# Kernel optimization log

Hardware: AMD Instinct MI355X
Metric: run time of the kernel (lower is better)

## Reference

```python
import jax, jax.numpy as jnp
import numpy as np

N_NODES = 100000
N_EDGES = 1600000
IN_DIM, HID_DIM, OUT_DIM = 256, 64, 64


def gcn_conv(x, src, dst, W, b, n_nodes):
    """PyG GCNConv: D^-1/2 (A + I) D^-1/2 X W + b (self-loops added, deg on dst)."""
    h = x @ W  # [N, D_out]
    ones = jnp.ones(src.shape[0], dtype=h.dtype)
    deg = jax.ops.segment_sum(ones, dst, num_segments=n_nodes) + 1.0  # +1 for self-loop
    dinv = jax.lax.rsqrt(deg)  # deg >= 1, always finite
    norm = dinv[src] * dinv[dst]  # [E]
    # neighbor aggregation (scatter-add) + self-loop contribution
    agg = jax.ops.segment_sum(h[src] * norm[:, None], dst, num_segments=n_nodes)
    agg = agg + h * (dinv * dinv)[:, None]
    return agg + b


def gcn_backbone(x, edge_index, W1, b1, W2, b2, n_nodes):
    src, dst = edge_index[0], edge_index[1]
    h = jax.nn.relu(gcn_conv(x, src, dst, W1, b1, n_nodes))
    h = gcn_conv(h, src, dst, W2, b2, n_nodes)
    return h


def zscore(h):
    # torch .std(0) is unbiased (ddof=1)
    return (h - h.mean(axis=0)) / jnp.std(h, axis=0, ddof=1)


def setup_inputs() -> dict:
    key = jax.random.key(0)
    k = jax.random.split(key, 8)
    x1 = jax.random.normal(k[0], (N_NODES, IN_DIM), dtype=jnp.float32)
    x2 = jax.random.normal(k[1], (N_NODES, IN_DIM), dtype=jnp.float32)
    edge_index1 = jax.random.randint(k[2], (2, N_EDGES), 0, N_NODES, dtype=jnp.int64)
    edge_index2 = jax.random.randint(k[3], (2, N_EDGES), 0, N_NODES, dtype=jnp.int64)
    W1 = jax.random.normal(k[4], (IN_DIM, HID_DIM), dtype=jnp.float32) * (1.0 / np.sqrt(IN_DIM))
    b1 = jnp.zeros((HID_DIM,), dtype=jnp.float32)
    W2 = jax.random.normal(k[5], (HID_DIM, OUT_DIM), dtype=jnp.float32) * (1.0 / np.sqrt(HID_DIM))
    b2 = jnp.zeros((OUT_DIM,), dtype=jnp.float32)
    return {"x1": x1, "edge_index1": edge_index1, "x2": x2, "edge_index2": edge_index2,
            "W1": W1, "b1": b1, "W2": W2, "b2": b2}


def reference(x1, edge_index1, x2, edge_index2, W1, b1, W2, b2):
    h1 = gcn_backbone(x1, edge_index1, W1, b1, W2, b2, N_NODES)
    h2 = gcn_backbone(x2, edge_index2, W1, b1, W2, b2, N_NODES)
    return zscore(h1), zscore(h2)
```

## Files before the change

### kernel.cpp

```cpp
#include <hip/hip_runtime.h>
#include <hip/hip_bf16.h>

#define HD 64
#define CH 8192
#define BKT_SHIFT 10
#define SRC_BITS 17
#define MAXBLK 256

typedef __attribute__((ext_vector_type(8))) short bf16x8;
typedef __attribute__((ext_vector_type(4))) float f32x4;
typedef __attribute__((ext_vector_type(4))) unsigned int u32x4;

#define WAITALL do { asm volatile("s_waitcnt vmcnt(0)" ::: "memory"); \
                     __builtin_amdgcn_sched_barrier(0); } while (0)

__device__ inline unsigned short f2bf(float x) {
  unsigned u = __float_as_uint(x);
  unsigned r = u + 0x7FFF + ((u >> 16) & 1);
  return (unsigned short)(r >> 16);
}
__device__ inline float bf2f(unsigned short h) {
  return __uint_as_float(((unsigned)h) << 16);
}

__global__ __launch_bounds__(256) void k_wprep(const float* __restrict__ W1,
                                               const float* __restrict__ W2,
                                               unsigned short* __restrict__ Wf1,
                                               unsigned short* __restrict__ Wf2hi,
                                               unsigned short* __restrict__ Wf2lo) {
  int idx = blockIdx.x * blockDim.x + threadIdx.x;
  if (idx < 256 * 64) {
    int k = idx >> 6, c = idx & 63;
    float w = W1[idx];
    int ks = k >> 5, r = k & 31, h2 = r >> 3, j = r & 7;
    int f = c >> 4, r16c = c & 15;
    int pos = (((ks * 4 + f) * 64) + h2 * 16 + r16c) * 8 + j;
    Wf1[pos] = f2bf(w);
  } else if (idx < 256 * 64 + 64 * 64) {
    int i2 = idx - 256 * 64;
    int k = i2 >> 6, c = i2 & 63;
    float w = W2[i2];
    int ks = k >> 5, r = k & 31, h2 = r >> 3, j = r & 7;
    int f = c >> 4, r16c = c & 15;
    int pos = (((ks * 4 + f) * 64) + h2 * 16 + r16c) * 8 + j;
    unsigned short hi = f2bf(w);
    Wf2hi[pos] = hi;
    Wf2lo[pos] = f2bf(w - bf2f(hi));
  }
}

__global__ __launch_bounds__(256) void k_front(
    const float* __restrict__ X0, const float* __restrict__ X1,
    const unsigned short* __restrict__ Wf1, unsigned short* __restrict__ Hb,
    int N, int gPer,
    const int* __restrict__ srcA, const int* __restrict__ dstA,
    const int* __restrict__ srcB, const int* __restrict__ dstB,
    int* __restrict__ tmp, int* __restrict__ counts, int* __restrict__ offsets,
    int NB, int NBLK, int E) {
  __shared__ int hist[128];
  __shared__ int pref[128];
  __shared__ int lofs[128];
  __shared__ int stage[CH];
  const int tid = threadIdx.x;
  const int bid = blockIdx.x;
  const int nGemm = 2 * gPer;

  if (bid < nGemm) {
    const int g = bid / gPer;
    const int bblk = bid % gPer;
    const float* __restrict__ Xv = g ? X1 : X0;
    const int lane = tid & 63;
    const int wv = tid >> 6;
    const int r16 = lane & 15;
    const int half = lane >> 4;
    const int row = bblk * 64 + wv * 16 + r16;
    const int rowc = min(row, N - 1);

    unsigned long long xa =
        (unsigned long long)(const void*)(Xv + (size_t)rowc * 256 + half * 8);
    f32x4 a[16];
    asm volatile(
        "global_load_dwordx4 %0, %16, off\n\t"
        "global_load_dwordx4 %1, %16, off offset:16\n\t"
        "global_load_dwordx4 %2, %16, off offset:128\n\t"
        "global_load_dwordx4 %3, %16, off offset:144\n\t"
        "global_load_dwordx4 %4, %16, off offset:256\n\t"
        "global_load_dwordx4 %5, %16, off offset:272\n\t"
        "global_load_dwordx4 %6, %16, off offset:384\n\t"
        "global_load_dwordx4 %7, %16, off offset:400\n\t"
        "global_load_dwordx4 %8, %16, off offset:512\n\t"
        "global_load_dwordx4 %9, %16, off offset:528\n\t"
        "global_load_dwordx4 %10, %16, off offset:640\n\t"
        "global_load_dwordx4 %11, %16, off offset:656\n\t"
        "global_load_dwordx4 %12, %16, off offset:768\n\t"
        "global_load_dwordx4 %13, %16, off offset:784\n\t"
        "global_load_dwordx4 %14, %16, off offset:896\n\t"
        "global_load_dwordx4 %15, %16, off offset:912\n\t"
        : "=&v"(a[0]), "=&v"(a[1]), "=&v"(a[2]), "=&v"(a[3]), "=&v"(a[4]),
          "=&v"(a[5]), "=&v"(a[6]), "=&v"(a[7]), "=&v"(a[8]), "=&v"(a[9]),
          "=&v"(a[10]), "=&v"(a[11]), "=&v"(a[12]), "=&v"(a[13]), "=&v"(a[14]),
          "=&v"(a[15])
        : "v"(xa));

    const unsigned long long wb = (unsigned long long)(const void*)Wf1 + lane * 16;
    bf16x8 B[32];
    asm volatile(
        "global_load_dwordx4 %0, %16, off\n\t"
        "global_load_dwordx4 %1, %16, off offset:1024\n\t"
        "global_load_dwordx4 %2, %16, off offset:2048\n\t"
        "global_load_dwordx4 %3, %16, off offset:3072\n\t"
        "global_load_dwordx4 %4, %17, off\n\t"
        "global_load_dwordx4 %5, %17, off offset:1024\n\t"
        "global_load_dwordx4 %6, %17, off offset:2048\n\t"
        "global_load_dwordx4 %7, %17, off offset:3072\n\t"
        "global_load_dwordx4 %8, %18, off\n\t"
        "global_load_dwordx4 %9, %18, off offset:1024\n\t"
        "global_load_dwordx4 %10, %18, off offset:2048\n\t"
        "global_load_dwordx4 %11, %18, off offset:3072\n\t"
        "global_load_dwordx4 %12, %19, off\n\t"
        "global_load_dwordx4 %13, %19, off offset:1024\n\t"
        "global_load_dwordx4 %14, %19, off offset:2048\n\t"
        "global_load_dwordx4 %15, %19, off offset:3072\n\t"
        : "=&v"(B[0]), "=&v"(B[1]), "=&v"(B[2]), "=&v"(B[3]), "=&v"(B[4]),
          "=&v"(B[5]), "=&v"(B[6]), "=&v"(B[7]), "=&v"(B[8]), "=&v"(B[9]),
          "=&v"(B[10]), "=&v"(B[11]), "=&v"(B[12]), "=&v"(B[13]), "=&v"(B[14]),
          "=&v"(B[15])
        : "v"(wb), "v"(wb + 4096), "v"(wb + 8192), "v"(wb + 12288));

    WAITALL;

    asm volatile(
        "global_load_dwordx4 %0, %16, off\n\t"
        "global_load_dwordx4 %1, %16, off offset:1024\n\t"
        "global_load_dwordx4 %2, %16, off offset:2048\n\t"
        "global_load_dwordx4 %3, %16, off offset:3072\n\t"
        "global_load_dwordx4 %4, %17, off\n\t"
        "global_load_dwordx4 %5, %17, off offset:1024\n\t"
        "global_load_dwordx4 %6, %17, off offset:2048\n\t"
        "global_load_dwordx4 %7, %17, off offset:3072\n\t"
        "global_load_dwordx4 %8, %18, off\n\t"
        "global_load_dwordx4 %9, %18, off offset:1024\n\t"
        "global_load_dwordx4 %10, %18, off offset:2048\n\t"
        "global_load_dwordx4 %11, %18, off offset:3072\n\t"
        "global_load_dwordx4 %12, %19, off\n\t"
        "global_load_dwordx4 %13, %19, off offset:1024\n\t"
        "global_load_dwordx4 %14, %19, off offset:2048\n\t"
        "global_load_dwordx4 %15, %19, off offset:3072\n\t"
        : "=&v"(B[16]), "=&v"(B[17]), "=&v"(B[18]), "=&v"(B[19]), "=&v"(B[20]),
          "=&v"(B[21]), "=&v"(B[22]), "=&v"(B[23]), "=&v"(B[24]), "=&v"(B[25]),
          "=&v"(B[26]), "=&v"(B[27]), "=&v"(B[28]), "=&v"(B[29]), "=&v"(B[30]),
          "=&v"(B[31])
        : "v"(wb + 16384), "v"(wb + 20480), "v"(wb + 24576), "v"(wb + 28672));

    f32x4 acc[4];
#pragma unroll
    for (int f = 0; f < 4; ++f) acc[f] = (f32x4){0.f, 0.f, 0.f, 0.f};

#pragma unroll
    for (int ks = 0; ks < 4; ++ks) {
      union { __hip_bfloat162 h[4]; bf16x8 v; } cu;
      cu.h[0] = __float22bfloat162_rn(make_float2(a[2 * ks][0], a[2 * ks][1]));
      cu.h[1] = __float22bfloat162_rn(make_float2(a[2 * ks][2], a[2 * ks][3]));
      cu.h[2] = __float22bfloat162_rn(make_float2(a[2 * ks + 1][0], a[2 * ks + 1][1]));
      cu.h[3] = __float22bfloat162_rn(make_float2(a[2 * ks + 1][2], a[2 * ks + 1][3]));
#pragma unroll
      for (int f = 0; f < 4; ++f)
        acc[f] = __builtin_amdgcn_mfma_f32_16x16x32_bf16(cu.v, B[ks * 4 + f], acc[f], 0, 0, 0);
    }

    WAITALL;

#pragma unroll
    for (int ks = 4; ks < 8; ++ks) {
      union { __hip_bfloat162 h[4]; bf16x8 v; } cu;
      cu.h[0] = __float22bfloat162_rn(make_float2(a[2 * ks][0], a[2 * ks][1]));
      cu.h[1] = __float22bfloat162_rn(make_float2(a[2 * ks][2], a[2 * ks][3]));
      cu.h[2] = __float22bfloat162_rn(make_float2(a[2 * ks + 1][0], a[2 * ks + 1][1]));
      cu.h[3] = __float22bfloat162_rn(make_float2(a[2 * ks + 1][2], a[2 * ks + 1][3]));
#pragma unroll
      for (int f = 0; f < 4; ++f)
        acc[f] = __builtin_amdgcn_mfma_f32_16x16x32_bf16(cu.v, B[ks * 4 + f], acc[f], 0, 0, 0);
    }

    const int orow0 = bblk * 64 + wv * 16 + half * 4;
#pragma unroll
    for (int f = 0; f < 4; ++f) {
#pragma unroll
      for (int rg = 0; rg < 4; ++rg) {
        int orow = orow0 + rg;
        if (orow < N) Hb[((size_t)g * N + orow) * HD + f * 16 + r16] = f2bf(acc[f][rg]);
      }
    }
    return;
  }

  const int blk2 = bid - nGemm;
  const int g = blk2 / NBLK;
  const int blk = blk2 % NBLK;
  const int* __restrict__ src = g ? srcB : srcA;
  const int* __restrict__ dst = g ? dstB : dstA;
  int* __restrict__ tmpg = tmp + (size_t)g * NBLK * CH;
  int* __restrict__ cntg = counts + (size_t)g * NB * NBLK;
  int* __restrict__ offg = offsets + (size_t)g * NB * NBLK;
  const int e0 = blk * CH;
  const int len = min(CH, E - e0);
  const int t = tid;

  for (int i = t; i < 128; i += 256) hist[i] = 0;
  __syncthreads();
  int dreg[CH / 256];
#pragma unroll
  for (int it = 0; it < CH / 256; ++it) {
    int i = t + it * 256;
    if (i < len) {
      int d = dst[e0 + i];
      dreg[it] = d;
      atomicAdd(&hist[d >> BKT_SHIFT], 1);
    }
  }
  __syncthreads();
  if (t < 128) pref[t] = hist[t];
  __syncthreads();
  for (int off = 1; off < 128; off <<= 1) {
    int v = 0;
    if (t < 128 && t >= off) v = pref[t - off];
    __syncthreads();
    if (t < 128) pref[t] += v;
    __syncthreads();
  }
  if (t < NB) {
    int ex = pref[t] - hist[t];
    lofs[t] = ex;
    cntg[t * NBLK + blk] = hist[t];
    offg[t * NBLK + blk] = ex;
  }
  __syncthreads();
#pragma unroll
  for (int it = 0; it < CH / 256; ++it) {
    int i = t + it * 256;
    if (i < len) {
      int d = dreg[it], s = src[e0 + i];
      int slot = atomicAdd(&lofs[d >> BKT_SHIFT], 1);
      stage[slot] = ((d & ((1 << BKT_SHIFT) - 1)) << SRC_BITS) | s;
    }
  }
  __syncthreads();
  int nv = len >> 2;
  for (int i = t; i < nv; i += 256) ((int4*)(tmpg + e0))[i] = ((const int4*)stage)[i];
  for (int i = (nv << 2) + t; i < len; i += 256) tmpg[e0 + i] = stage[i];
}

__global__ __launch_bounds__(128) void k_bscan(const int* __restrict__ counts,
                                               int* __restrict__ bucket_base,
                                               int* __restrict__ row_start,
                                               int NB, int NBLK, int N, int E) {
  __shared__ int sh[128];
  const int g = blockIdx.x;
  const int* __restrict__ cntg = counts + (size_t)g * NB * NBLK;
  int* __restrict__ bbg = bucket_base + g * (NB + 1);
  int* __restrict__ rsg = row_start + (size_t)g * (N + 1);
  int t = threadIdx.x;
  int v = 0;
  if (t < NB) {
    const int* p = cntg + t * NBLK;
    for (int i = 0; i < NBLK; ++i) v += p[i];
  }
  sh[t] = v;
  __syncthreads();
  for (int off = 1; off < 128; off <<= 1) {
    int x = (t >= off) ? sh[t - off] : 0;
    __syncthreads();
    sh[t] += x;
    __syncthreads();
  }
  if (t < NB) bbg[t] = sh[t] - v;
  if (t == 0) {
    bbg[NB] = E;
    rsg[N] = E;
  }
}

__global__ __launch_bounds__(1024) void k_bin2m(const int* __restrict__ tmp,
                                                const int* __restrict__ counts,
                                                const int* __restrict__ offsets,
                                                const int* __restrict__ bucket_base,
                                                int* __restrict__ row_start,
                                                float* __restrict__ dinv,
                                                int* __restrict__ recs, int N, int NB,
                                                int NBLK, int E) {
  __shared__ int h[1 << BKT_SHIFT];
  __shared__ int lcur[1 << BKT_SHIFT];
  __shared__ int scnt[MAXBLK], soff[MAXBLK];
  const int g = blockIdx.x / NB;
  const int b = blockIdx.x % NB;
  const int* __restrict__ tmpg = tmp + (size_t)g * NBLK * CH;
  const int* __restrict__ cntg = counts + (size_t)g * NB * NBLK;
  const int* __restrict__ offg = offsets + (size_t)g * NB * NBLK;
  const int* __restrict__ bbg = bucket_base + g * (NB + 1);
  int* __restrict__ rsg = row_start + (size_t)g * (N + 1);
  float* __restrict__ dig = dinv + (size_t)g * N;
  int* __restrict__ recg = recs + (size_t)g * E;
  const int t = threadIdx.x;
  const int node0 = b << BKT_SHIFT;
  const int lane = t & 63, w = t >> 6;

  h[t] = 0;
  for (int i = t; i < NBLK; i += 1024) {
    scnt[i] = cntg[b * NBLK + i];
    soff[i] = offg[b * NBLK + i];
  }
  __syncthreads();
  for (int blk = w; blk < NBLK; blk += 16) {
    int cnt = scnt[blk];
    const int* p = tmpg + blk * CH + soff[blk];
    for (int j = lane; j < cnt; j += 64) atomicAdd(&h[p[j] >> SRC_BITS], 1);
  }
  __syncthreads();
  int deg = h[t];
  __syncthreads();
  for (int off = 1; off < 1024; off <<= 1) {
    int x = (t >= off) ? h[t - off] : 0;
    __syncthreads();
    h[t] += x;
    __syncthreads();
  }
  int base = bbg[b] + h[t] - deg;
  lcur[t] = base;
  int n = node0 + t;
  if (n < N) {
    rsg[n] = base;
    dig[n] = rsqrtf((float)deg + 1.0f);
  }
  __syncthreads();
  for (int blk = w; blk < NBLK; blk += 16) {
    int cnt = scnt[blk];
    const int* p = tmpg + blk * CH + soff[blk];
    for (int j = lane; j < cnt; j += 64) {
      int rec = p[j];
      int d = rec >> SRC_BITS;
      int s = rec & ((1 << SRC_BITS) - 1);
      int slot = atomicAdd(&lcur[d], 1);
      recg[slot] = s;
    }
  }
}

__global__ __launch_bounds__(256) void k_gemm2(const unsigned short* __restrict__ Xb,
                                               const unsigned short* __restrict__ Wfh,
                                               const unsigned short* __restrict__ Wfl,
                                               unsigned short* __restrict__ Hb, int M) {
  const int tid = threadIdx.x;
  const int row0 = blockIdx.x * 64;
  const int lane = tid & 63;
  const int wv = tid >> 6;
  const int r16 = lane & 15;
  const int half = lane >> 4;
  const int row = row0 + wv * 16 + r16;
  const int rowc = min(row, M - 1);

  unsigned long long xa =
      (unsigned long long)(const void*)(Xb + (size_t)rowc * 64 + half * 8);
  const unsigned long long bh = (unsigned long long)(const void*)Wfh + lane * 16;
  const unsigned long long bl = (unsigned long long)(const void*)Wfl + lane * 16;
  u32x4 A0, A1;
  bf16x8 BH[8], BL[8];
  asm volatile(
      "global_load_dwordx4 %0, %18, off\n\t"
      "global_load_dwordx4 %1, %18, off offset:64\n\t"
      "global_load_dwordx4 %2, %19, off\n\t"
      "global_load_dwordx4 %3, %19, off offset:1024\n\t"
      "global_load_dwordx4 %4, %19, off offset:2048\n\t"
      "global_load_dwordx4 %5, %19, off offset:3072\n\t"
      "global_load_dwordx4 %6, %20, off\n\t"
      "global_load_dwordx4 %7, %20, off offset:1024\n\t"
      "global_load_dwordx4 %8, %20, off offset:2048\n\t"
      "global_load_dwordx4 %9, %20, off offset:3072\n\t"
      "global_load_dwordx4 %10, %21, off\n\t"
      "global_load_dwordx4 %11, %21, off offset:1024\n\t"
      "global_load_dwordx4 %12, %21, off offset:2048\n\t"
      "global_load_dwordx4 %13, %21, off offset:3072\n\t"
      "global_load_dwordx4 %14, %22, off\n\t"
      "global_load_dwordx4 %15, %22, off offset:1024\n\t"
      "global_load_dwordx4 %16, %22, off offset:2048\n\t"
      "global_load_dwordx4 %17, %22, off offset:3072\n\t"
      : "=&v"(A0), "=&v"(A1), "=&v"(BH[0]), "=&v"(BH[1]), "=&v"(BH[2]),
        "=&v"(BH[3]), "=&v"(BH[4]), "=&v"(BH[5]), "=&v"(BH[6]), "=&v"(BH[7]),
        "=&v"(BL[0]), "=&v"(BL[1]), "=&v"(BL[2]), "=&v"(BL[3]), "=&v"(BL[4]),
        "=&v"(BL[5]), "=&v"(BL[6]), "=&v"(BL[7])
      : "v"(xa), "v"(bh), "v"(bh + 4096), "v"(bl), "v"(bl + 4096));

  WAITALL;

  f32x4 acc[4];
#pragma unroll
  for (int f = 0; f < 4; ++f) acc[f] = (f32x4){0.f, 0.f, 0.f, 0.f};

  union { u32x4 u; bf16x8 v; } a0u, a1u;
  a0u.u = A0;
  a1u.u = A1;
#pragma unroll
  for (int f = 0; f < 4; ++f) {
    acc[f] = __builtin_amdgcn_mfma_f32_16x16x32_bf16(a0u.v, BH[f], acc[f], 0, 0, 0);
    acc[f] = __builtin_amdgcn_mfma_f32_16x16x32_bf16(a0u.v, BL[f], acc[f], 0, 0, 0);
    acc[f] = __builtin_amdgcn_mfma_f32_16x16x32_bf16(a1u.v, BH[4 + f], acc[f], 0, 0, 0);
    acc[f] = __builtin_amdgcn_mfma_f32_16x16x32_bf16(a1u.v, BL[4 + f], acc[f], 0, 0, 0);
  }

  const int orow0 = row0 + wv * 16 + half * 4;
#pragma unroll
  for (int f = 0; f < 4; ++f) {
#pragma unroll
    for (int rg = 0; rg < 4; ++rg) {
      int orow = orow0 + rg;
      if (orow < M) Hb[(size_t)orow * HD + f * 16 + r16] = f2bf(acc[f][rg]);
    }
  }
}

template <int OUTBF16>
__global__ __launch_bounds__(256) void k_agg(const unsigned short* __restrict__ Hb,
                                             const int* __restrict__ recs,
                                             const int* __restrict__ row_start,
                                             const float* __restrict__ dinv,
                                             const float* __restrict__ bias,
                                             void* __restrict__ outv, int N, int E,
                                             int relu) {
  const int t = threadIdx.x;
  const int nglob = (blockIdx.x * blockDim.x + t) >> 4;
  const int lane16 = t & 15;
  if (nglob >= 2 * N) return;
  const int g = nglob >= N;
  const int node = nglob - g * N;
  const int* __restrict__ rsg = row_start + (size_t)g * (N + 1);
  const int* __restrict__ R = recs + (size_t)g * E;
  const float* __restrict__ dig = dinv + (size_t)g * N;
  const unsigned short* __restrict__ Hbg = Hb + (size_t)g * N * HD;

  const int c0 = lane16 * 4;
  float di = dig[node];
  float a0, a1, a2, a3;
  {
    uint2 h = *(const uint2*)&Hbg[(size_t)node * HD + c0];
    float dd = di * di;
    a0 = bf2f((unsigned short)(h.x & 0xffff)) * dd;
    a1 = bf2f((unsigned short)(h.x >> 16)) * dd;
    a2 = bf2f((unsigned short)(h.y & 0xffff)) * dd;
    a3 = bf2f((unsigned short)(h.y >> 16)) * dd;
  }
  const int beg = rsg[node], end = rsg[node + 1];
  int e = beg;
  for (; e + 8 <= end; e += 8) {
    int s[8];
    uint2 gg[8];
    float n[8];
#pragma unroll
    for (int j = 0; j < 8; ++j) s[j] = R[e + j];
#pragma unroll
    for (int j = 0; j < 8; ++j) {
      gg[j] = *(const uint2*)&Hbg[(size_t)s[j] * HD + c0];
      n[j] = dig[s[j]];
    }
#pragma unroll
    for (int j = 0; j < 8; ++j) {
      float nn = n[j] * di;
      a0 = fmaf(bf2f((unsigned short)(gg[j].x & 0xffff)), nn, a0);
      a1 = fmaf(bf2f((unsigned short)(gg[j].x >> 16)), nn, a1);
      a2 = fmaf(bf2f((unsigned short)(gg[j].y & 0xffff)), nn, a2);
      a3 = fmaf(bf2f((unsigned short)(gg[j].y >> 16)), nn, a3);
    }
  }
  for (; e < end; ++e) {
    int s = R[e];
    uint2 gg = *(const uint2*)&Hbg[(size_t)s * HD + c0];
    float nn = dig[s] * di;
    a0 = fmaf(bf2f((unsigned short)(gg.x & 0xffff)), nn, a0);
    a1 = fmaf(bf2f((unsigned short)(gg.x >> 16)), nn, a1);
    a2 = fmaf(bf2f((unsigned short)(gg.y & 0xffff)), nn, a2);
    a3 = fmaf(bf2f((unsigned short)(gg.y >> 16)), nn, a3);
  }
  float4 bv = *(const float4*)&bias[c0];
  a0 += bv.x; a1 += bv.y; a2 += bv.z; a3 += bv.w;
  if (relu) {
    a0 = fmaxf(a0, 0.f); a1 = fmaxf(a1, 0.f);
    a2 = fmaxf(a2, 0.f); a3 = fmaxf(a3, 0.f);
  }
  if (OUTBF16) {
    uint2 o;
    o.x = ((unsigned)f2bf(a1) << 16) | f2bf(a0);
    o.y = ((unsigned)f2bf(a3) << 16) | f2bf(a2);
    *(uint2*)&((unsigned short*)outv)[(size_t)nglob * HD + c0] = o;
  } else {
    *(float4*)&((float*)outv)[(size_t)nglob * HD + c0] = make_float4(a0, a1, a2, a3);
  }
}


__global__ void k_colstats(const float* __restrict__ H, float* __restrict__ stats, int N,
                           int gridPer) {
  __shared__ float ss[256], sq[256];
  const int g = blockIdx.x / gridPer;
  const int blk = blockIdx.x % gridPer;
  const float* __restrict__ Hg = H + (size_t)g * N * HD;
  float* __restrict__ st = stats + g * 128;
  int t = threadIdx.x;
  int col = t & 63, grp = t >> 6;
  float s = 0.f, q = 0.f;
  for (int row = blk * 4 + grp; row < N; row += gridPer * 4) {
    float v = Hg[(size_t)row * HD + col];
    s += v;
    q += v * v;
  }
  ss[t] = s;
  sq[t] = q;
  __syncthreads();
  if (t < 64) {
    s = ss[t] + ss[t + 64] + ss[t + 128] + ss[t + 192];
    q = sq[t] + sq[t + 64] + sq[t + 128] + sq[t + 192];
    atomicAdd(&st[t], s);
    atomicAdd(&st[64 + t], q);
  }
}

__global__ void k_normalize(float* __restrict__ H, const float* __restrict__ stats, int N) {
  int i = blockIdx.x * blockDim.x + threadIdx.x;
  int total = 2 * N * HD;
  if (i >= total) return;
  int col = i & 63;
  const float* st = stats + (i >= N * HD ? 128 : 0);
  float sum = st[col], sumsq = st[64 + col];
  float mean = sum / (float)N;
  float var = (sumsq - sum * sum / (float)N) / (float)(N - 1);
  float r = rsqrtf(var);
  H[i] = (H[i] - mean) * r;
}


extern "C" void kernel_launch(void* const* d_in, const int* in_sizes, int n_in,
                              void* d_out, int out_size, void* d_ws, size_t ws_size,
                              hipStream_t stream) {
  const int IN_DIM = 256;
  const float* X1 = (const float*)d_in[0];
  const float* X2 = (const float*)d_in[2];
  const int* EI1 = (const int*)d_in[1];
  const int* EI2 = (const int*)d_in[3];
  const float* W1 = (const float*)d_in[4];
  const float* b1 = (const float*)d_in[5];
  const float* W2 = (const float*)d_in[6];
  const float* b2 = (const float*)d_in[7];
  const int N = in_sizes[0] / IN_DIM;
  const int E = in_sizes[1] / 2;
  const int NB = (N + (1 << BKT_SHIFT) - 1) >> BKT_SHIFT;
  const int NBLK = (E + CH - 1) / CH;

  char* ws = (char*)d_ws;
  size_t off = 0;
  auto carve = [&](size_t bytes) -> char* {
    char* p = ws + off;
    off += (bytes + 255) & ~(size_t)255;
    return p;
  };
  unsigned short* Hb = (unsigned short*)carve((size_t)2 * N * HD * 2);
  int* tmp = (int*)carve((size_t)2 * NBLK * CH * 4);
  int* recs = (int*)carve((size_t)2 * E * 4);
  char* zero_base = carve(256 * 4);
  float* stats = (float*)zero_base;
  int* row_start = (int*)carve((size_t)2 * (N + 1) * 4);
  float* dinv = (float*)carve((size_t)2 * N * 4);
  int* bucket_base = (int*)carve((size_t)2 * (NB + 1) * 4);
  int* counts = (int*)carve((size_t)2 * NB * NBLK * 4);
  int* offsets = (int*)carve((size_t)2 * NB * NBLK * 4);
  unsigned short* Wf1 = (unsigned short*)carve(256 * 64 * 2);
  unsigned short* Wf2hi = (unsigned short*)carve(64 * 64 * 2);
  unsigned short* Wf2lo = (unsigned short*)carve(64 * 64 * 2);
  unsigned short* bufAgg = (unsigned short*)d_out;
  (void)ws_size; (void)n_in; (void)out_size;

  const int T = 256;
  const int gPer1 = (N + 63) / 64;
  const int gG2 = (2 * N + 63) / 64;
  const int gAgg = (2 * N * 16 + T - 1) / T;
  const int gCS = 512;
  const int gElem = (2 * N * HD + T - 1) / T;
  const int gWp = (256 * 64 + 64 * 64 + T - 1) / T;

  (void)hipMemsetAsync(zero_base, 0, 256 * 4, stream);
  k_wprep<<<gWp, T, 0, stream>>>(W1, W2, Wf1, Wf2hi, Wf2lo);
  k_front<<<2 * gPer1 + 2 * NBLK, T, 0, stream>>>(X1, X2, Wf1, Hb, N, gPer1,
                                                  EI1, EI1 + E, EI2, EI2 + E,
                                                  tmp, counts, offsets, NB, NBLK, E);
  k_bscan<<<2, 128, 0, stream>>>(counts, bucket_base, row_start, NB, NBLK, N, E);
  k_bin2m<<<2 * NB, 1024, 0, stream>>>(tmp, counts, offsets, bucket_base, row_start,
                                       dinv, recs, N, NB, NBLK, E);

  k_agg<1><<<gAgg, T, 0, stream>>>(Hb, recs, row_start, dinv, b1, bufAgg, N, E, 1);
  k_gemm2<<<gG2, T, 0, stream>>>(bufAgg, Wf2hi, Wf2lo, Hb, 2 * N);
  k_agg<0><<<gAgg, T, 0, stream>>>(Hb, recs, row_start, dinv, b2, d_out, N, E, 0);

  k_colstats<<<2 * gCS, T, 0, stream>>>((float*)d_out, stats, N, gCS);
  k_normalize<<<gElem, T, 0, stream>>>((float*)d_out, stats, N);
}
```

Measured before the change: 364.3 us.

## Fuse column statistics into the final aggregation and interleave GEMM with binning blocks

The separate column-statistics kernel is removed. The second aggregation kernel now accumulates per-column sums and sums of squares in shared memory with atomics, then flushes them to global stats once per block. This avoids a full re-read of the fp32 output. The front kernel also interleaves edge-binning blocks among the GEMM blocks, one in every eight, instead of placing them after all GEMM blocks, so the memory-bound binning runs alongside the compute-heavy GEMM. The cost is shared-memory atomic contention and an extra barrier in the aggregation kernel.

```diff
diff --git a/kernel.cpp b/kernel.cpp
--- a/kernel.cpp
+++ b/kernel.cpp
@@ -63,11 +63,15 @@
   __shared__ int stage[CH];
   const int tid = threadIdx.x;
   const int bid = blockIdx.x;
-  const int nGemm = 2 * gPer;
-
-  if (bid < nGemm) {
-    const int g = bid / gPer;
-    const int bblk = bid % gPer;
+  const int nBin = 2 * NBLK;
+
+  const int q = bid >> 3, r8 = bid & 7;
+  const bool isBin = (r8 == 7) && (q < nBin);
+
+  if (!isBin) {
+    const int gemmIdx = bid - min(nBin, (bid + 1) >> 3);
+    const int g = gemmIdx / gPer;
+    const int bblk = gemmIdx % gPer;
     const float* __restrict__ Xv = g ? X1 : X0;
     const int lane = tid & 63;
     const int wv = tid >> 6;
@@ -194,9 +198,8 @@
     return;
   }
 
-  const int blk2 = bid - nGemm;
-  const int g = blk2 / NBLK;
-  const int blk = blk2 % NBLK;
+  const int g = q / NBLK;
+  const int blk = q % NBLK;
   const int* __restrict__ src = g ? srcB : srcA;
   const int* __restrict__ dst = g ? dstB : dstA;
   int* __restrict__ tmpg = tmp + (size_t)g * NBLK * CH;
@@ -417,109 +420,107 @@
   }
 }
 
-template <int OUTBF16>
+template <int OUTBF16, int STATS>
 __global__ __launch_bounds__(256) void k_agg(const unsigned short* __restrict__ Hb,
                                              const int* __restrict__ recs,
                                              const int* __restrict__ row_start,
                                              const float* __restrict__ dinv,
                                              const float* __restrict__ bias,
-                                             void* __restrict__ outv, int N, int E,
+                                             void* __restrict__ outv,
+                                             float* __restrict__ stats, int N, int E,
                                              int relu) {
+  __shared__ float ssum[STATS ? 64 : 1], ssq[STATS ? 64 : 1];
   const int t = threadIdx.x;
   const int nglob = (blockIdx.x * blockDim.x + t) >> 4;
   const int lane16 = t & 15;
-  if (nglob >= 2 * N) return;
-  const int g = nglob >= N;
-  const int node = nglob - g * N;
+  const bool active = (nglob < 2 * N);
+  const int g = active ? (nglob >= N) : 0;
+  const int node = active ? (nglob - g * N) : 0;
   const int* __restrict__ rsg = row_start + (size_t)g * (N + 1);
   const int* __restrict__ R = recs + (size_t)g * E;
   const float* __restrict__ dig = dinv + (size_t)g * N;
   const unsigned short* __restrict__ Hbg = Hb + (size_t)g * N * HD;
 
+  if (STATS) {
+    if (t < 64) { ssum[t] = 0.f; ssq[t] = 0.f; }
+    __syncthreads();
+  }
+
   const int c0 = lane16 * 4;
-  float di = dig[node];
-  float a0, a1, a2, a3;
-  {
-    uint2 h = *(const uint2*)&Hbg[(size_t)node * HD + c0];
-    float dd = di * di;
-    a0 = bf2f((unsigned short)(h.x & 0xffff)) * dd;
-    a1 = bf2f((unsigned short)(h.x >> 16)) * dd;
-    a2 = bf2f((unsigned short)(h.y & 0xffff)) * dd;
-    a3 = bf2f((unsigned short)(h.y >> 16)) * dd;
-  }
-  const int beg = rsg[node], end = rsg[node + 1];
-  int e = beg;
-  for (; e + 8 <= end; e += 8) {
-    int s[8];
-    uint2 gg[8];
-    float n[8];
-#pragma unroll
-    for (int j = 0; j < 8; ++j) s[j] = R[e + j];
-#pragma unroll
-    for (int j = 0; j < 8; ++j) {
-      gg[j] = *(const uint2*)&Hbg[(size_t)s[j] * HD + c0];
-      n[j] = dig[s[j]];
-    }
-#pragma unroll
-    for (int j = 0; j < 8; ++j) {
-      float nn = n[j] * di;
-      a0 = fmaf(bf2f((unsigned short)(gg[j].x & 0xffff)), nn, a0);
-      a1 = fmaf(bf2f((unsigned short)(gg[j].x >> 16)), nn, a1);
-      a2 = fmaf(bf2f((unsigned short)(gg[j].y & 0xffff)), nn, a2);
-      a3 = fmaf(bf2f((unsigned short)(gg[j].y >> 16)), nn, a3);
-    }
-  }
-  for (; e < end; ++e) {
-    int s = R[e];
-    uint2 gg = *(const uint2*)&Hbg[(size_t)s * HD + c0];
-    float nn = dig[s] * di;
-    a0 = fmaf(bf2f((unsigned short)(gg.x & 0xffff)), nn, a0);
-    a1 = fmaf(bf2f((unsigned short)(gg.x >> 16)), nn, a1);
-    a2 = fmaf(bf2f((unsigned short)(gg.y & 0xffff)), nn, a2);
-    a3 = fmaf(bf2f((unsigned short)(gg.y >> 16)), nn, a3);
-  }
-  float4 bv = *(const float4*)&bias[c0];
-  a0 += bv.x; a1 += bv.y; a2 += bv.z; a3 += bv.w;
-  if (relu) {
-    a0 = fmaxf(a0, 0.f); a1 = fmaxf(a1, 0.f);
-    a2 = fmaxf(a2, 0.f); a3 = fmaxf(a3, 0.f);
-  }
-  if (OUTBF16) {
-    uint2 o;
-    o.x = ((unsigned)f2bf(a1) << 16) | f2bf(a0);
-    o.y = ((unsigned)f2bf(a3) << 16) | f2bf(a2);
-    *(uint2*)&((unsigned short*)outv)[(size_t)nglob * HD + c0] = o;
-  } else {
-    *(float4*)&((float*)outv)[(size_t)nglob * HD + c0] = make_float4(a0, a1, a2, a3);
-  }
-}
-
-
-__global__ void k_colstats(const float* __restrict__ H, float* __restrict__ stats, int N,
-                           int gridPer) {
-  __shared__ float ss[256], sq[256];
-  const int g = blockIdx.x / gridPer;
-  const int blk = blockIdx.x % gridPer;
-  const float* __restrict__ Hg = H + (size_t)g * N * HD;
-  float* __restrict__ st = stats + g * 128;
-  int t = threadIdx.x;
-  int col = t & 63, grp = t >> 6;
-  float s = 0.f, q = 0.f;
-  for (int row = blk * 4 + grp; row < N; row += gridPer * 4) {
-    float v = Hg[(size_t)row * HD + col];
-    s += v;
-    q += v * v;
-  }
-  ss[t] = s;
-  sq[t] = q;
-  __syncthreads();
-  if (t < 64) {
-    s = ss[t] + ss[t + 64] + ss[t + 128] + ss[t + 192];
-    q = sq[t] + sq[t + 64] + sq[t + 128] + sq[t + 192];
-    atomicAdd(&st[t], s);
-    atomicAdd(&st[64 + t], q);
-  }
-}
+  float a0 = 0.f, a1 = 0.f, a2 = 0.f, a3 = 0.f;
+  if (active) {
+    float di = dig[node];
+    {
+      uint2 h = *(const uint2*)&Hbg[(size_t)node * HD + c0];
+      float dd = di * di;
+      a0 = bf2f((unsigned short)(h.x & 0xffff)) * dd;
+      a1 = bf2f((unsigned short)(h.x >> 16)) * dd;
+      a2 = bf2f((unsigned short)(h.y & 0xffff)) * dd;
+      a3 = bf2f((unsigned short)(h.y >> 16)) * dd;
+    }
+    const int beg = rsg[node], end = rsg[node + 1];
+    int e = beg;
+    for (; e + 8 <= end; e += 8) {
+      int s[8];
+      uint2 gg[8];
+      float n[8];
+#pragma unroll
+      for (int j = 0; j < 8; ++j) s[j] = R[e + j];
+#pragma unroll
+      for (int j = 0; j < 8; ++j) {
+        gg[j] = *(const uint2*)&Hbg[(size_t)s[j] * HD + c0];
+        n[j] = dig[s[j]];
+      }
+#pragma unroll
+      for (int j = 0; j < 8; ++j) {
+        float nn = n[j] * di;
+        a0 = fmaf(bf2f((unsigned short)(gg[j].x & 0xffff)), nn, a0);
+        a1 = fmaf(bf2f((unsigned short)(gg[j].x >> 16)), nn, a1);
+        a2 = fmaf(bf2f((unsigned short)(gg[j].y & 0xffff)), nn, a2);
+        a3 = fmaf(bf2f((unsigned short)(gg[j].y >> 16)), nn, a3);
+      }
+    }
+    for (; e < end; ++e) {
+      int s = R[e];
+      uint2 gg = *(const uint2*)&Hbg[(size_t)s * HD + c0];
+      float nn = dig[s] * di;
+      a0 = fmaf(bf2f((unsigned short)(gg.x & 0xffff)), nn, a0);
+      a1 = fmaf(bf2f((unsigned short)(gg.x >> 16)), nn, a1);
+      a2 = fmaf(bf2f((unsigned short)(gg.y & 0xffff)), nn, a2);
+      a3 = fmaf(bf2f((unsigned short)(gg.y >> 16)), nn, a3);
+    }
+    float4 bv = *(const float4*)&bias[c0];
+    a0 += bv.x; a1 += bv.y; a2 += bv.z; a3 += bv.w;
+    if (relu) {
+      a0 = fmaxf(a0, 0.f); a1 = fmaxf(a1, 0.f);
+      a2 = fmaxf(a2, 0.f); a3 = fmaxf(a3, 0.f);
+    }
+    if (OUTBF16) {
+      uint2 o;
+      o.x = ((unsigned)f2bf(a1) << 16) | f2bf(a0);
+      o.y = ((unsigned)f2bf(a3) << 16) | f2bf(a2);
+      *(uint2*)&((unsigned short*)outv)[(size_t)nglob * HD + c0] = o;
+    } else {
+      *(float4*)&((float*)outv)[(size_t)nglob * HD + c0] = make_float4(a0, a1, a2, a3);
+    }
+  }
+
+  if (STATS) {
+    if (active) {
+      atomicAdd(&ssum[c0 + 0], a0); atomicAdd(&ssum[c0 + 1], a1);
+      atomicAdd(&ssum[c0 + 2], a2); atomicAdd(&ssum[c0 + 3], a3);
+      atomicAdd(&ssq[c0 + 0], a0 * a0); atomicAdd(&ssq[c0 + 1], a1 * a1);
+      atomicAdd(&ssq[c0 + 2], a2 * a2); atomicAdd(&ssq[c0 + 3], a3 * a3);
+    }
+    __syncthreads();
+    if (t < 64 && active) {
+      float* st = stats + g * 128;
+      atomicAdd(&st[t], ssum[t]);
+      atomicAdd(&st[64 + t], ssq[t]);
+    }
+  }
+}
+
 
 __global__ void k_normalize(float* __restrict__ H, const float* __restrict__ stats, int N) {
   int i = blockIdx.x * blockDim.x + threadIdx.x;
@@ -577,25 +578,27 @@
 
   const int T = 256;
   const int gPer1 = (N + 63) / 64;
+  const int nGemm = 2 * gPer1;
+  const int nBin = 2 * NBLK;
   const int gG2 = (2 * N + 63) / 64;
   const int gAgg = (2 * N * 16 + T - 1) / T;
-  const int gCS = 512;
   const int gElem = (2 * N * HD + T - 1) / T;
   const int gWp = (256 * 64 + 64 * 64 + T - 1) / T;
 
   (void)hipMemsetAsync(zero_base, 0, 256 * 4, stream);
   k_wprep<<<gWp, T, 0, stream>>>(W1, W2, Wf1, Wf2hi, Wf2lo);
-  k_front<<<2 * gPer1 + 2 * NBLK, T, 0, stream>>>(X1, X2, Wf1, Hb, N, gPer1,
-                                                  EI1, EI1 + E, EI2, EI2 + E,
-                                                  tmp, counts, offsets, NB, NBLK, E);
+  k_front<<<nGemm + nBin, T, 0, stream>>>(X1, X2, Wf1, Hb, N, gPer1,
+                                          EI1, EI1 + E, EI2, EI2 + E,
+                                          tmp, counts, offsets, NB, NBLK, E);
   k_bscan<<<2, 128, 0, stream>>>(counts, bucket_base, row_start, NB, NBLK, N, E);
   k_bin2m<<<2 * NB, 1024, 0, stream>>>(tmp, counts, offsets, bucket_base, row_start,
                                        dinv, recs, N, NB, NBLK, E);
 
-  k_agg<1><<<gAgg, T, 0, stream>>>(Hb, recs, row_start, dinv, b1, bufAgg, N, E, 1);
+  k_agg<1, 0><<<gAgg, T, 0, stream>>>(Hb, recs, row_start, dinv, b1, bufAgg, nullptr,
+                                      N, E, 1);
   k_gemm2<<<gG2, T, 0, stream>>>(bufAgg, Wf2hi, Wf2lo, Hb, 2 * N);
-  k_agg<0><<<gAgg, T, 0, stream>>>(Hb, recs, row_start, dinv, b2, d_out, N, E, 0);
-
-  k_colstats<<<2 * gCS, T, 0, stream>>>((float*)d_out, stats, N, gCS);
+  k_agg<0, 1><<<gAgg, T, 0, stream>>>(Hb, recs, row_start, dinv, b2, d_out, stats,
+                                      N, E, 0);
+
   k_normalize<<<gElem, T, 0, stream>>>((float*)d_out, stats, N);
 }
```

Result: slower. 675.2 us (+85.4%).
